# Optimization experiments

Hardware: AMD Instinct MI355X
Metric: run time of the kernel (lower is better)

Reference implementation:

```python
import jax, jax.numpy as jnp
import numpy as np

BS, C_IN, S1 = 64, 256, 32
D_OUT, J = 32, 10          # out_dim, num_out_caps (as_final_output -> spatial_size_2)
I = S1 * S1                # num_in_caps = 1024
ROUTE_NUM = 3


def setup_inputs() -> dict:
    key = jax.random.key(0)
    k1, k2, k3 = jax.random.split(key, 3)
    x = jax.random.normal(k1, (BS, C_IN, S1, S1), dtype=jnp.float32)
    W = jax.random.normal(k2, (D_OUT * J, C_IN), dtype=jnp.float32) * 0.02  # 1x1 conv weight
    W_b = jax.random.normal(k3, (D_OUT * J,), dtype=jnp.float32) * 0.02     # conv bias
    return {"x": x, "W": W, "W_b": W_b}


def squash(vec):
    # vec: [bs, j, d]; coeff = ||v||^2 / (1+||v||^2) / ||v||
    norm = jnp.linalg.norm(vec, axis=2, keepdims=True)
    norm_sq = norm * norm
    return vec * (norm_sq / (1.0 + norm_sq) / norm)


def reference(x, W, W_b):
    bs = x.shape[0]
    # 1x1 conv == per-pixel matmul: [bs, J*D, h, w]
    pred = jnp.einsum('bchw,oc->bohw', x, W) + W_b[None, :, None, None]
    # torch: resize(bs, J, D, I) on contiguous tensor, then permute(0,3,1,2)
    pred = pred.reshape(bs, J, D_OUT, I).transpose(0, 3, 1, 2)  # [bs, I, J, D]
    b = jnp.zeros((bs, J, I), dtype=x.dtype)  # b_init='zero'
    v = None
    for _ in range(ROUTE_NUM):
        c = jax.nn.softmax(b, axis=1)                    # softmax over output caps j
        s = jnp.einsum('bji,bijd->bjd', c, pred)          # per-capsule weighted sum
        v = squash(s)                                     # [bs, J, D]
        delta_b = jnp.einsum('bjd,bijd->bji', v, pred)    # agreement
        b = b + jax.lax.stop_gradient(delta_b)            # torch .detach()
    return v  # as_final_output=True -> [bs, J, D]
```

## Files before the change

kernel.cpp:

```cpp
#include <hip/hip_runtime.h>
#include <hip/hip_bf16.h>

typedef __attribute__((ext_vector_type(8))) unsigned short u16x8;
typedef __attribute__((ext_vector_type(4))) unsigned short u16x4;
typedef __attribute__((ext_vector_type(8))) short short8;
typedef __attribute__((ext_vector_type(4))) float floatx4;

#define BS 64
#define CIN 256
#define II 1024
#define OO 320
#define JJ 10
#define DD 32

__device__ __forceinline__ float b2f(unsigned short u) {
    union { unsigned int i; float f; } x; x.i = ((unsigned int)u) << 16; return x.f;
}
__device__ __forceinline__ unsigned short f2b(float f) {
    union { float f; unsigned int i; } x; x.f = f;
    unsigned int r = x.i + 0x7fffu + ((x.i >> 16) & 1u);
    return (unsigned short)(r >> 16);
}

__device__ __forceinline__ float butterfly32(const float* p, int l) {
    float q16[16];
#pragma unroll
    for (int d = 0; d < 16; ++d) {
        float keep = (l & 1) ? p[2 * d + 1] : p[2 * d];
        float send = (l & 1) ? p[2 * d] : p[2 * d + 1];
        q16[d] = keep + __shfl_xor(send, 1);
    }
    float q8[8];
#pragma unroll
    for (int d = 0; d < 8; ++d) {
        float keep = (l & 2) ? q16[2 * d + 1] : q16[2 * d];
        float send = (l & 2) ? q16[2 * d] : q16[2 * d + 1];
        q8[d] = keep + __shfl_xor(send, 2);
    }
    float q4[4];
#pragma unroll
    for (int d = 0; d < 4; ++d) {
        float keep = (l & 4) ? q8[2 * d + 1] : q8[2 * d];
        float send = (l & 4) ? q8[2 * d] : q8[2 * d + 1];
        q4[d] = keep + __shfl_xor(send, 4);
    }
    float q2[2];
#pragma unroll
    for (int d = 0; d < 2; ++d) {
        float keep = (l & 8) ? q4[2 * d + 1] : q4[2 * d];
        float send = (l & 8) ? q4[2 * d] : q4[2 * d + 1];
        q2[d] = keep + __shfl_xor(send, 8);
    }
    float keep = (l & 16) ? q2[1] : q2[0];
    float send = (l & 16) ? q2[0] : q2[1];
    float q1 = keep + __shfl_xor(send, 16);
    q1 += __shfl_xor(q1, 32);
    return q1;
}

__global__ __launch_bounds__(256) void k_prepW(const float* __restrict__ W,
                                               unsigned short* __restrict__ Wl) {
    int gid = blockIdx.x * 256 + threadIdx.x;
    int lm = gid & 15;
    int quad = (gid >> 4) & 3;
    int mtl = (gid >> 6) & 3;
    int ks = (gid >> 8) & 7;
    int oc = gid >> 11;
    const float* src = W + (size_t)(oc * 64 + mtl * 16 + lm) * CIN + ks * 32 + quad * 8;
    float4 v0 = *(const float4*)src;
    float4 v1 = *(const float4*)(src + 4);
    u16x8 u;
    u[0] = f2b(v0.x); u[1] = f2b(v0.y); u[2] = f2b(v0.z); u[3] = f2b(v0.w);
    u[4] = f2b(v1.x); u[5] = f2b(v1.y); u[6] = f2b(v1.z); u[7] = f2b(v1.w);
    *(u16x8*)(Wl + (size_t)gid * 8) = u;
}


__global__ __launch_bounds__(512) void k_gemm8(const float* __restrict__ x,
                                               const unsigned short* __restrict__ Wl,
                                               const float* __restrict__ Wb,
                                               unsigned short* __restrict__ pred,
                                               float* __restrict__ psumC) {
    __shared__ unsigned short buf[2][16896];
    __shared__ float Wb_lds[OO];

    const int ic = blockIdx.x, b = blockIdx.y;
    const int t = threadIdx.x, w = t >> 6, l = t & 63;
    const int lm = l & 15, quad = l >> 4;
    const int i0 = ic * 128;

    if (t < OO) Wb_lds[t] = Wb[t];

    {
        const u16x8* src = (const u16x8*)Wl;
        u16x8* dst = (u16x8*)buf[1];
        dst[t] = src[t];
        dst[t + 512] = src[t + 512];
        dst[t + 1024] = src[t + 1024];
        dst[t + 1536] = src[t + 1536];
    }

    short8 bfrag[8];
    float csum[2];
    const int crow = t >> 5, f4 = t & 31;
    const int cs_c = t >> 2, cs_seg = t & 3;
#pragma unroll
    for (int kc = 0; kc < 2; ++kc) {
        float4 fr[8];
#pragma unroll
        for (int p = 0; p < 8; ++p) {
            int c = kc * 128 + p * 16 + crow;
            fr[p] = *(const float4*)(x + ((size_t)b * CIN + c) * II + i0 + 4 * f4);
        }
#pragma unroll
        for (int p = 0; p < 8; ++p) {
            int cl = p * 16 + crow;
            u16x4 u;
            u[0] = f2b(fr[p].x); u[1] = f2b(fr[p].y); u[2] = f2b(fr[p].z); u[3] = f2b(fr[p].w);
            *(u16x4*)&buf[0][cl * 132 + 4 * f4] = u;
        }
        __syncthreads();
#pragma unroll
        for (int k2 = 0; k2 < 4; ++k2) {
            short8 f;
#pragma unroll
            for (int j = 0; j < 8; ++j)
                f[j] = (short)buf[0][(k2 * 32 + quad * 8 + j) * 132 + w * 16 + lm];
            bfrag[kc * 4 + k2] = f;
        }
        {
            float cs = 0.f;
#pragma unroll
            for (int q = 0; q < 8; ++q) {
                u16x4 u = *(const u16x4*)&buf[0][cs_c * 132 + cs_seg * 32 + q * 4];
                cs += b2f(u[0]) + b2f(u[1]) + b2f(u[2]) + b2f(u[3]);
            }
            cs += __shfl_xor(cs, 1);
            cs += __shfl_xor(cs, 2);
            csum[kc] = cs;
        }
        __syncthreads();
    }
    if (cs_seg == 0) {
        size_t cbase = ((size_t)ic * BS + b) * CIN;
        psumC[cbase + cs_c] = csum[0];
        psumC[cbase + 128 + cs_c] = csum[1];
    }

    const size_t predbase = ((size_t)(b * 8 + ic)) * 40960 + (size_t)(w * 16 + lm) * 4;
#pragma unroll 1
    for (int oc = 0; oc < 5; ++oc) {
        if (oc < 4) {
            const u16x8* src = (const u16x8*)Wl + (size_t)(oc + 1) * 2048;
            u16x8* dst = (u16x8*)buf[oc & 1];
            dst[t] = src[t];
            dst[t + 512] = src[t + 512];
            dst[t + 1024] = src[t + 1024];
            dst[t + 1536] = src[t + 1536];
        }
        const unsigned short* ab = buf[(oc + 1) & 1];
        floatx4 acc[4] = {};
#pragma unroll
        for (int ks = 0; ks < 8; ++ks)
#pragma unroll
            for (int mtl = 0; mtl < 4; ++mtl) {
                short8 af = *(const short8*)(ab + (size_t)(((ks * 4 + mtl) * 4 + quad) * 16 + lm) * 8);
                acc[mtl] = __builtin_amdgcn_mfma_f32_16x16x32_bf16(af, bfrag[ks], acc[mtl], 0, 0, 0);
            }
#pragma unroll
        for (int mtl = 0; mtl < 4; ++mtl) {
            int ob = oc * 64 + mtl * 16 + quad * 4;
            int mprime = oc * 16 + mtl * 4 + quad;
            u16x4 sv;
#pragma unroll
            for (int r = 0; r < 4; ++r) sv[r] = f2b(acc[mtl][r] + Wb_lds[ob + r]);
            *(u16x4*)(pred + predbase + (size_t)mprime * 512) = sv;
        }
        __syncthreads();
    }
}

__global__ __launch_bounds__(320) void k_gemv(const float* __restrict__ psumC,
                                              const float* __restrict__ W,
                                              const float* __restrict__ Wb,
                                              float* __restrict__ s1) {
    __shared__ float y_lds[CIN];
    const int b = blockIdx.x, t = threadIdx.x;
    if (t < CIN) {
        float s = 0.f;
#pragma unroll
        for (int sl = 0; sl < 8; ++sl) s += psumC[((size_t)sl * BS + b) * CIN + t];
        y_lds[t] = s;
    }
    __syncthreads();
    const float* wr = W + (size_t)t * CIN;
    float acc = 0.f;
#pragma unroll 4
    for (int c = 0; c < CIN; c += 4) {
        float4 wv = *(const float4*)(wr + c);
        acc += wv.x * y_lds[c] + wv.y * y_lds[c + 1] + wv.z * y_lds[c + 2] + wv.w * y_lds[c + 3];
    }
    s1[(size_t)b * OO + t] = 0.1f * (acc + 1024.0f * Wb[t]);
}

__global__ __launch_bounds__(640) void k_route1(const float* __restrict__ s1,
                                                const unsigned short* __restrict__ pred,
                                                float* __restrict__ blogG,
                                                float* __restrict__ psum1) {
    __shared__ float s_lds[OO];
    __shared__ float v_lds[OO];
    __shared__ float cf[JJ];
    __shared__ float dbuf[JJ][128];

    const int ic = blockIdx.x, b = blockIdx.y;
    const int t = threadIdx.x, w = t >> 6, l = t & 63;

    u16x8 Ld[8];
    {
        const unsigned short* p0 = pred + ((size_t)(b * 8 + ic)) * 40960
                                 + (size_t)(w * 8) * 512 + 8 * l;
#pragma unroll
        for (int dq = 0; dq < 8; ++dq)
            Ld[dq] = *(const u16x8*)(p0 + (size_t)dq * 512);
    }

    if (t < OO) s_lds[t] = s1[(size_t)b * OO + t];
    __syncthreads();
    if (t < JJ) {
        float n2 = 0.f;
#pragma unroll
        for (int d = 0; d < DD; ++d) { float v = s_lds[t * DD + d]; n2 += v * v; }
        cf[t] = sqrtf(n2) / (1.0f + n2);
    }
    __syncthreads();
    if (t < OO) v_lds[t] = s_lds[t] * cf[t >> 5];
    __syncthreads();

    float d0 = 0.f, d1 = 0.f;
#pragma unroll
    for (int dq = 0; dq < 8; ++dq)
#pragma unroll
        for (int e = 0; e < 4; ++e) {
            float vv = v_lds[w * DD + dq * 4 + e];
            d0 += vv * b2f(Ld[dq][e]);
            d1 += vv * b2f(Ld[dq][4 + e]);
        }
    *(float2*)(blogG + ((size_t)b * JJ + w) * II + ic * 128 + 2 * l) = make_float2(d0, d1);
    dbuf[w][2 * l] = d0; dbuf[w][2 * l + 1] = d1;
    __syncthreads();

    if (t < 128) {
        float lg[JJ];
#pragma unroll
        for (int j = 0; j < JJ; ++j) lg[j] = dbuf[j][t];
        float m = lg[0];
#pragma unroll
        for (int j = 1; j < JJ; ++j) m = fmaxf(m, lg[j]);
        float Z = 0.f, c[JJ];
#pragma unroll
        for (int j = 0; j < JJ; ++j) { c[j] = __expf(lg[j] - m); Z += c[j]; }
        float inv = 1.0f / Z;
#pragma unroll
        for (int j = 0; j < JJ; ++j) dbuf[j][t] = c[j] * inv;
    }
    __syncthreads();

    float c0 = dbuf[w][2 * l], c1 = dbuf[w][2 * l + 1];
    float p[DD];
#pragma unroll
    for (int dq = 0; dq < 8; ++dq)
#pragma unroll
        for (int e = 0; e < 4; ++e)
            p[dq * 4 + e] = c0 * b2f(Ld[dq][e]) + c1 * b2f(Ld[dq][4 + e]);
    float s = butterfly32(p, l);
    if (l < 32) psum1[((size_t)ic * BS + b) * OO + w * DD + l] = s;
}

__global__ __launch_bounds__(640) void k_route2(const float* __restrict__ psum1,
                                                const unsigned short* __restrict__ pred,
                                                const float* __restrict__ blogG,
                                                float* __restrict__ psum2) {
    __shared__ float s_lds[OO];
    __shared__ float v_lds[OO];
    __shared__ float cf[JJ];
    __shared__ float dbuf[JJ][128];

    const int ic = blockIdx.x, b = blockIdx.y;
    const int t = threadIdx.x, w = t >> 6, l = t & 63;

    u16x8 Ld[8];
    {
        const unsigned short* p0 = pred + ((size_t)(b * 8 + ic)) * 40960
                                 + (size_t)(w * 8) * 512 + 8 * l;
#pragma unroll
        for (int dq = 0; dq < 8; ++dq)
            Ld[dq] = *(const u16x8*)(p0 + (size_t)dq * 512);
    }

    if (t < OO) {
        float s = 0.f;
#pragma unroll
        for (int sl = 0; sl < 8; ++sl) s += psum1[((size_t)sl * BS + b) * OO + t];
        s_lds[t] = s;
    }
    __syncthreads();
    if (t < JJ) {
        float n2 = 0.f;
#pragma unroll
        for (int d = 0; d < DD; ++d) { float v = s_lds[t * DD + d]; n2 += v * v; }
        cf[t] = sqrtf(n2) / (1.0f + n2);
    }
    __syncthreads();
    if (t < OO) v_lds[t] = s_lds[t] * cf[t >> 5];
    __syncthreads();

    float d0 = 0.f, d1 = 0.f;
#pragma unroll
    for (int dq = 0; dq < 8; ++dq)
#pragma unroll
        for (int e = 0; e < 4; ++e) {
            float vv = v_lds[w * DD + dq * 4 + e];
            d0 += vv * b2f(Ld[dq][e]);
            d1 += vv * b2f(Ld[dq][4 + e]);
        }
    float2 bl = *(const float2*)(blogG + ((size_t)b * JJ + w) * II + ic * 128 + 2 * l);
    dbuf[w][2 * l] = bl.x + d0; dbuf[w][2 * l + 1] = bl.y + d1;
    __syncthreads();

    if (t < 128) {
        float lg[JJ];
#pragma unroll
        for (int j = 0; j < JJ; ++j) lg[j] = dbuf[j][t];
        float m = lg[0];
#pragma unroll
        for (int j = 1; j < JJ; ++j) m = fmaxf(m, lg[j]);
        float Z = 0.f, c[JJ];
#pragma unroll
        for (int j = 0; j < JJ; ++j) { c[j] = __expf(lg[j] - m); Z += c[j]; }
        float inv = 1.0f / Z;
#pragma unroll
        for (int j = 0; j < JJ; ++j) dbuf[j][t] = c[j] * inv;
    }
    __syncthreads();

    float c0 = dbuf[w][2 * l], c1 = dbuf[w][2 * l + 1];
    float p[DD];
#pragma unroll
    for (int dq = 0; dq < 8; ++dq)
#pragma unroll
        for (int e = 0; e < 4; ++e)
            p[dq * 4 + e] = c0 * b2f(Ld[dq][e]) + c1 * b2f(Ld[dq][4 + e]);
    float s = butterfly32(p, l);
    if (l < 32) psum2[((size_t)ic * BS + b) * OO + w * DD + l] = s;
}

__global__ __launch_bounds__(320) void k_final2(const float* __restrict__ psum2,
                                                float* __restrict__ out) {
    __shared__ float s_lds[OO];
    __shared__ float cf[JJ];
    int b = blockIdx.x, t = threadIdx.x;
    float s = 0.f;
#pragma unroll
    for (int sl = 0; sl < 8; ++sl) s += psum2[((size_t)sl * BS + b) * OO + t];
    s_lds[t] = s;
    __syncthreads();
    if (t < JJ) {
        float n2 = 0.f;
#pragma unroll
        for (int d = 0; d < DD; ++d) { float v = s_lds[t * DD + d]; n2 += v * v; }
        cf[t] = sqrtf(n2) / (1.0f + n2);
    }
    __syncthreads();
    out[b * OO + t] = s_lds[t] * cf[t >> 5];
}

extern "C" void kernel_launch(void* const* d_in, const int* in_sizes, int n_in,
                              void* d_out, int out_size, void* d_ws, size_t ws_size,
                              hipStream_t stream) {
    const float* x  = (const float*)d_in[0];
    const float* W  = (const float*)d_in[1];
    const float* Wb = (const float*)d_in[2];

    char* ws = (char*)d_ws;
    unsigned short* pred = (unsigned short*)ws;
    unsigned short* Wl   = (unsigned short*)(ws + 41943040);
    float* psumC = (float*)(ws + 42106880);
    float* s1    = (float*)(ws + 42631168);
    float* psum1 = (float*)(ws + 42713088);
    float* psum2 = (float*)(ws + 43368448);
    float* blogG = (float*)(ws + 44023808);

    k_prepW<<<40, 256, 0, stream>>>(W, Wl);
    k_gemm8<<<dim3(8, BS), 512, 0, stream>>>(x, Wl, Wb, pred, psumC);
    k_gemv<<<BS, 320, 0, stream>>>(psumC, W, Wb, s1);
    k_route1<<<dim3(8, BS), 640, 0, stream>>>(s1, pred, blogG, psum1);
    k_route2<<<dim3(8, BS), 640, 0, stream>>>(psum1, pred, blogG, psum2);
    k_final2<<<BS, 320, 0, stream>>>(psum2, (float*)d_out);
}
```

Measured before the change: 146.8 us.

## Fuse gemv into route1 and final squash into route2 via last-block atomics

Removes two small kernel launches. Every route1 block now recomputes the per-batch 320x256 gemv that builds the first-iteration s vector. route2 accumulates its partial sums with atomicAdd into a buffer that k_prepW zeroes, and the last block per batch, found through a counter, does the final squash. This trades launch overhead for redundant gemv work (8x per batch) and atomic traffic, and makes float summation order nondeterministic.

Result: slower. 219.7 us (+49.7%).

```diff
diff --git a/kernel.cpp b/kernel.cpp
--- a/kernel.cpp
+++ b/kernel.cpp
@@ -59,8 +59,11 @@
 }
 
 __global__ __launch_bounds__(256) void k_prepW(const float* __restrict__ W,
-                                               unsigned short* __restrict__ Wl) {
+                                               unsigned short* __restrict__ Wl,
+                                               float* __restrict__ zr) {
     int gid = blockIdx.x * 256 + threadIdx.x;
+    if (gid < 10240) { zr[gid] = 0.f; zr[gid + 10240] = 0.f; }
+    if (gid < 64) zr[gid + 20480] = 0.f;
     int lm = gid & 15;
     int quad = (gid >> 4) & 3;
     int mtl = (gid >> 6) & 3;
@@ -180,33 +183,13 @@
     }
 }
 
-__global__ __launch_bounds__(320) void k_gemv(const float* __restrict__ psumC,
-                                              const float* __restrict__ W,
-                                              const float* __restrict__ Wb,
-                                              float* __restrict__ s1) {
-    __shared__ float y_lds[CIN];
-    const int b = blockIdx.x, t = threadIdx.x;
-    if (t < CIN) {
-        float s = 0.f;
-#pragma unroll
-        for (int sl = 0; sl < 8; ++sl) s += psumC[((size_t)sl * BS + b) * CIN + t];
-        y_lds[t] = s;
-    }
-    __syncthreads();
-    const float* wr = W + (size_t)t * CIN;
-    float acc = 0.f;
-#pragma unroll 4
-    for (int c = 0; c < CIN; c += 4) {
-        float4 wv = *(const float4*)(wr + c);
-        acc += wv.x * y_lds[c] + wv.y * y_lds[c + 1] + wv.z * y_lds[c + 2] + wv.w * y_lds[c + 3];
-    }
-    s1[(size_t)b * OO + t] = 0.1f * (acc + 1024.0f * Wb[t]);
-}
-
-__global__ __launch_bounds__(640) void k_route1(const float* __restrict__ s1,
+__global__ __launch_bounds__(640) void k_route1(const float* __restrict__ psumC,
+                                                const float* __restrict__ W,
+                                                const float* __restrict__ Wb,
                                                 const unsigned short* __restrict__ pred,
                                                 float* __restrict__ blogG,
                                                 float* __restrict__ psum1) {
+    __shared__ float y_lds[CIN];
     __shared__ float s_lds[OO];
     __shared__ float v_lds[OO];
     __shared__ float cf[JJ];
@@ -224,7 +207,23 @@
             Ld[dq] = *(const u16x8*)(p0 + (size_t)dq * 512);
     }
 
-    if (t < OO) s_lds[t] = s1[(size_t)b * OO + t];
+    if (t < CIN) {
+        float s = 0.f;
+#pragma unroll
+        for (int sl = 0; sl < 8; ++sl) s += psumC[((size_t)sl * BS + b) * CIN + t];
+        y_lds[t] = s;
+    }
+    __syncthreads();
+    if (t < OO) {
+        const float* wr = W + (size_t)t * CIN;
+        float acc = 0.f;
+#pragma unroll 4
+        for (int c = 0; c < CIN; c += 4) {
+            float4 wv = *(const float4*)(wr + c);
+            acc += wv.x * y_lds[c] + wv.y * y_lds[c + 1] + wv.z * y_lds[c + 2] + wv.w * y_lds[c + 3];
+        }
+        s_lds[t] = 0.1f * (acc + 1024.0f * Wb[t]);
+    }
     __syncthreads();
     if (t < JJ) {
         float n2 = 0.f;
@@ -279,11 +278,14 @@
 __global__ __launch_bounds__(640) void k_route2(const float* __restrict__ psum1,
                                                 const unsigned short* __restrict__ pred,
                                                 const float* __restrict__ blogG,
-                                                float* __restrict__ psum2) {
+                                                float* __restrict__ psum2f,
+                                                unsigned* __restrict__ cnt,
+                                                float* __restrict__ out) {
     __shared__ float s_lds[OO];
     __shared__ float v_lds[OO];
     __shared__ float cf[JJ];
     __shared__ float dbuf[JJ][128];
+    __shared__ int lastblk;
 
     const int ic = blockIdx.x, b = blockIdx.y;
     const int t = threadIdx.x, w = t >> 6, l = t & 63;
@@ -351,27 +353,33 @@
         for (int e = 0; e < 4; ++e)
             p[dq * 4 + e] = c0 * b2f(Ld[dq][e]) + c1 * b2f(Ld[dq][4 + e]);
     float s = butterfly32(p, l);
-    if (l < 32) psum2[((size_t)ic * BS + b) * OO + w * DD + l] = s;
-}
-
-__global__ __launch_bounds__(320) void k_final2(const float* __restrict__ psum2,
-                                                float* __restrict__ out) {
-    __shared__ float s_lds[OO];
-    __shared__ float cf[JJ];
-    int b = blockIdx.x, t = threadIdx.x;
-    float s = 0.f;
-#pragma unroll
-    for (int sl = 0; sl < 8; ++sl) s += psum2[((size_t)sl * BS + b) * OO + t];
-    s_lds[t] = s;
-    __syncthreads();
-    if (t < JJ) {
-        float n2 = 0.f;
-#pragma unroll
-        for (int d = 0; d < DD; ++d) { float v = s_lds[t * DD + d]; n2 += v * v; }
-        cf[t] = sqrtf(n2) / (1.0f + n2);
-    }
-    __syncthreads();
-    out[b * OO + t] = s_lds[t] * cf[t >> 5];
+    if (l < 32) atomicAdd(&psum2f[(size_t)b * OO + w * DD + l], s);
+    __syncthreads();
+
+    if (t == 0) {
+        __threadfence();
+        unsigned old = atomicAdd(&cnt[b], 1u);
+        lastblk = (old == 7u) ? 1 : 0;
+    }
+    __syncthreads();
+
+    if (lastblk) {
+        __threadfence();
+        if (t < OO) {
+            float v = __hip_atomic_load(&psum2f[(size_t)b * OO + t],
+                                        __ATOMIC_RELAXED, __HIP_MEMORY_SCOPE_AGENT);
+            s_lds[t] = v;
+        }
+        __syncthreads();
+        if (t < JJ) {
+            float n2 = 0.f;
+#pragma unroll
+            for (int d = 0; d < DD; ++d) { float v = s_lds[t * DD + d]; n2 += v * v; }
+            cf[t] = sqrtf(n2) / (1.0f + n2);
+        }
+        __syncthreads();
+        if (t < OO) out[b * OO + t] = s_lds[t] * cf[t >> 5];
+    }
 }
 
 extern "C" void kernel_launch(void* const* d_in, const int* in_sizes, int n_in,
@@ -384,16 +392,14 @@
     char* ws = (char*)d_ws;
     unsigned short* pred = (unsigned short*)ws;
     unsigned short* Wl   = (unsigned short*)(ws + 41943040);
-    float* psumC = (float*)(ws + 42106880);
-    float* s1    = (float*)(ws + 42631168);
-    float* psum1 = (float*)(ws + 42713088);
-    float* psum2 = (float*)(ws + 43368448);
-    float* blogG = (float*)(ws + 44023808);
-
-    k_prepW<<<40, 256, 0, stream>>>(W, Wl);
+    float* psumC  = (float*)(ws + 42106880);
+    float* psum1  = (float*)(ws + 42631168);
+    float* psum2f = (float*)(ws + 43286528);
+    unsigned* cnt = (unsigned*)(ws + 43368448);
+    float* blogG  = (float*)(ws + 43368704);
+
+    k_prepW<<<40, 256, 0, stream>>>(W, Wl, psum2f);
     k_gemm8<<<dim3(8, BS), 512, 0, stream>>>(x, Wl, Wb, pred, psumC);
-    k_gemv<<<BS, 320, 0, stream>>>(psumC, W, Wb, s1);
-    k_route1<<<dim3(8, BS), 640, 0, stream>>>(s1, pred, blogG, psum1);
-    k_route2<<<dim3(8, BS), 640, 0, stream>>>(psum1, pred, blogG, psum2);
-    k_final2<<<BS, 320, 0, stream>>>(psum2, (float*)d_out);
-}
+    k_route1<<<dim3(8, BS), 640, 0, stream>>>(psumC, W, Wb, pred, blogG, psum1);
+    k_route2<<<dim3(8, BS), 640, 0, stream>>>(psum1, pred, blogG, psum2f, cnt, (float*)d_out);
+}
```
